# Kernel tuning notes

Hardware: AMD Instinct MI355X
Metric: run time of the kernel (lower is better)

## Reference

```python
import jax, jax.numpy as jnp
import numpy as np

KERNEL = 16
STRIDE = 16


def _coverage_1d(length, k, s):
    # Count, per position, how many sliding windows (start = g*s, size k) cover it.
    # This reproduces F.fold(F.unfold(ones)) which the torch module uses to build
    # its mask; positions never covered by any window become 0 -> masked out.
    n_win = (length - k) // s + 1
    idx = (jnp.arange(n_win) * s)[:, None] + jnp.arange(k)  # [n_win, k]
    return jnp.zeros((length,), dtype=jnp.float32).at[idx.reshape(-1)].add(1.0)


def setup_inputs() -> dict:
    key = jax.random.key(0)
    x = jax.random.normal(key, (2, 3, 224, 224), dtype=jnp.float32)
    return {"x": x}


def reference(x):
    # Faithful to the torch module: the constructed mask is the fold of unfolded
    # ones, which (crucially) does NOT vary with the window index p -- the expand
    # along dim 3 is uniform. So mask[n, p, c, h, w] = (coverage(h, w) > 0).
    # Output: x broadcast to [N, p, C, H, W], zeroed where coverage == 0.
    if x.ndim == 3:
        x = x[None]
    N, C, H, W = x.shape
    ph = (H - KERNEL) // STRIDE + 1
    pw = (W - KERNEL) // STRIDE + 1
    p = ph * pw
    cov = _coverage_1d(H, KERNEL, STRIDE)[:, None] * _coverage_1d(W, KERNEL, STRIDE)[None, :]
    mask = cov > 0  # [H, W]
    out = jnp.where(mask, x[:, None], jnp.zeros((), dtype=x.dtype))  # [N,1,C,H,W]
    return jnp.broadcast_to(out, (N, p, C, H, W))
```

## Files before the change

### kernel.cpp

```cpp
#include <hip/hip_runtime.h>


namespace {
constexpr int N = 2, C = 3, H = 224, W = 224;
constexpr int PH = (H - 16) / 16 + 1;
constexpr int PW = (W - 16) / 16 + 1;
constexpr int P  = PH * PW;
constexpr int CHW_VEC = C * H * W / 4;
constexpr int TOTAL_VEC = N * P * CHW_VEC;
}

__global__ __launch_bounds__(256) void wm_broadcast_kernel(
    const float4* __restrict__ x, float4* __restrict__ out) {
  int stride = gridDim.x * blockDim.x;
  for (int i = blockIdx.x * blockDim.x + threadIdx.x; i < TOTAL_VEC; i += stride) {
    int np_idx = i / CHW_VEC;
    int chw    = i - np_idx * CHW_VEC;
    int n      = np_idx / P;
    out[i] = x[n * CHW_VEC + chw];
  }
}

extern "C" void kernel_launch(void* const* d_in, const int* in_sizes, int n_in,
                              void* d_out, int out_size, void* d_ws, size_t ws_size,
                              hipStream_t stream) {
  const float4* x = (const float4*)d_in[0];
  float4* out = (float4*)d_out;
  int blocks = 4096;
  wm_broadcast_kernel<<<blocks, 256, 0, stream>>>(x, out);
}
```

Baseline: 42.28 us.

## Load each input vector once and write 28 patch copies with nontemporal stores

Each thread now loads one float4 of x and stores it to 28 consecutive patch slots. This replaces the grid-stride loop in which every output element re-read x and paid integer divides. Stores use nontemporal hints to avoid polluting the cache on this write-heavy broadcast of about 117 MB. The launch is sized exactly (N*CHW_VEC*7 threads), and the exact division by 256 relies on the fixed shapes.

```diff
diff --git a/kernel.cpp b/kernel.cpp
--- a/kernel.cpp
+++ b/kernel.cpp
@@ -2,30 +2,35 @@
 
 
 namespace {
+typedef float f32x4 __attribute__((ext_vector_type(4)));
+
 constexpr int N = 2, C = 3, H = 224, W = 224;
-constexpr int PH = (H - 16) / 16 + 1;
-constexpr int PW = (W - 16) / 16 + 1;
-constexpr int P  = PH * PW;
+constexpr int P = ((H - 16) / 16 + 1) * ((W - 16) / 16 + 1);
 constexpr int CHW_VEC = C * H * W / 4;
-constexpr int TOTAL_VEC = N * P * CHW_VEC;
+constexpr int PGRP = 28;
+constexpr int NPG = P / PGRP;
+constexpr int TOTAL_THREADS = N * CHW_VEC * NPG;
 }
 
-__global__ __launch_bounds__(256) void wm_broadcast_kernel(
-    const float4* __restrict__ x, float4* __restrict__ out) {
-  int stride = gridDim.x * blockDim.x;
-  for (int i = blockIdx.x * blockDim.x + threadIdx.x; i < TOTAL_VEC; i += stride) {
-    int np_idx = i / CHW_VEC;
-    int chw    = i - np_idx * CHW_VEC;
-    int n      = np_idx / P;
-    out[i] = x[n * CHW_VEC + chw];
+__global__ __launch_bounds__(256) void wm_bcast_kernel(
+    const f32x4* __restrict__ x, f32x4* __restrict__ out) {
+  int tid = blockIdx.x * 256 + threadIdx.x;
+  int pg  = tid / (N * CHW_VEC);
+  int rem = tid - pg * (N * CHW_VEC);
+  int n   = rem / CHW_VEC;
+  int chw = rem - n * CHW_VEC;
+  f32x4 v = x[n * CHW_VEC + chw];
+  int base = (n * P + pg * PGRP) * CHW_VEC + chw;
+#pragma unroll
+  for (int k = 0; k < PGRP; ++k) {
+    __builtin_nontemporal_store(v, &out[base + k * CHW_VEC]);
   }
 }
 
 extern "C" void kernel_launch(void* const* d_in, const int* in_sizes, int n_in,
                               void* d_out, int out_size, void* d_ws, size_t ws_size,
                               hipStream_t stream) {
-  const float4* x = (const float4*)d_in[0];
-  float4* out = (float4*)d_out;
-  int blocks = 4096;
-  wm_broadcast_kernel<<<blocks, 256, 0, stream>>>(x, out);
+  const f32x4* x = (const f32x4*)d_in[0];
+  f32x4* out = (f32x4*)d_out;
+  wm_bcast_kernel<<<TOTAL_THREADS / 256, 256, 0, stream>>>(x, out);
 }
```

After: 46.21 us. 1.09x slower.
